# Optimization experiments

Hardware: AMD Instinct MI355X
Metric: run time of the kernel (lower is better)

## Reference

```python
import jax, jax.numpy as jnp
from jax import lax
import numpy as np

PRE_NMS_TOPN = 2000
POST_NMS_TOPN = 300
NMS_IOU_THRESHOLD = 0.7
EPS = 1e-8


def setup_inputs() -> dict:
    key = jax.random.key(0)
    k1, k2 = jax.random.split(key, 2)
    B, H, W, A = 64, 100, 100, 9
    # small-magnitude deltas so exp(dh/dw) stays sane, as real RPN outputs do
    rpn_bbox_deltas = jax.random.normal(k1, (B, H, W, A * 4), dtype=jnp.float32) * 0.1
    rpn_labels = jax.random.uniform(k2, (B, H, W, A), dtype=jnp.float32)
    # grid anchors, normalized coords, 3 scales x 3 ratios = 9 per position
    ys = (jnp.arange(H, dtype=jnp.float32) + 0.5) / H
    xs = (jnp.arange(W, dtype=jnp.float32) + 0.5) / W
    scales = jnp.array([0.1, 0.2, 0.4], dtype=jnp.float32)
    ratios = jnp.array([0.5, 1.0, 2.0], dtype=jnp.float32)
    hh = (scales[:, None] * jnp.sqrt(ratios)[None, :]).reshape(-1)  # [9]
    ww = (scales[:, None] / jnp.sqrt(ratios)[None, :]).reshape(-1)  # [9]
    cy, cx = jnp.meshgrid(ys, xs, indexing="ij")  # [H,W]
    cy, cx = cy[..., None], cx[..., None]         # [H,W,1]
    anchors = jnp.stack(
        [cy - hh / 2, cx - ww / 2, cy + hh / 2, cx + ww / 2], axis=-1
    ).reshape(-1, 4)  # [H*W*9, 4] = [90000, 4]
    return {"rpn_bbox_deltas": rpn_bbox_deltas, "rpn_labels": rpn_labels, "anchors": anchors}


def _decode_deltas(anchors, deltas):
    # anchors [N,4] (y1,x1,y2,x2), deltas [B,N,4] (dy,dx,dh,dw)
    anc_h = anchors[:, 2] - anchors[:, 0]
    anc_w = anchors[:, 3] - anchors[:, 1]
    anc_cy = anchors[:, 0] + 0.5 * anc_h
    anc_cx = anchors[:, 1] + 0.5 * anc_w
    h = jnp.exp(deltas[..., 2]) * anc_h
    w = jnp.exp(deltas[..., 3]) * anc_w
    cy = deltas[..., 0] * anc_h + anc_cy
    cx = deltas[..., 1] * anc_w + anc_cx
    y1 = cy - 0.5 * h
    x1 = cx - 0.5 * w
    return jnp.stack([y1, x1, y1 + h, x1 + w], axis=-1)  # [B,N,4]


def _nms_single(boxes):
    # boxes [PRE,4] already sorted by score descending; greedy hard NMS
    n = boxes.shape[0]
    area = jnp.maximum(boxes[:, 2] - boxes[:, 0], 0.0) * jnp.maximum(boxes[:, 3] - boxes[:, 1], 0.0)
    idx = jnp.arange(n)

    def body(i, keep):
        b = boxes[i]
        yy1 = jnp.maximum(b[0], boxes[:, 0])
        xx1 = jnp.maximum(b[1], boxes[:, 1])
        yy2 = jnp.minimum(b[2], boxes[:, 2])
        xx2 = jnp.minimum(b[3], boxes[:, 3])
        inter = jnp.maximum(yy2 - yy1, 0.0) * jnp.maximum(xx2 - xx1, 0.0)
        iou = inter / (area[i] + area - inter + EPS)
        suppress = (iou > NMS_IOU_THRESHOLD) & (idx > i) & keep[i]
        return keep & ~suppress

    keep = lax.fori_loop(0, n, body, jnp.ones((n,), dtype=bool))
    # compact kept boxes (score order) into fixed [POST,4], zero-padded
    pos = jnp.where(keep, jnp.cumsum(keep) - 1, POST_NMS_TOPN)
    pos = jnp.minimum(pos, POST_NMS_TOPN)
    out = jnp.zeros((POST_NMS_TOPN + 1, 4), dtype=boxes.dtype).at[pos].set(boxes)[:POST_NMS_TOPN]
    return jnp.clip(out, 0.0, 1.0)  # clip_boxes=True in tf combined NMS


def reference(rpn_bbox_deltas, rpn_labels, anchors):
    B = rpn_bbox_deltas.shape[0]
    N = anchors.shape[0]
    deltas = rpn_bbox_deltas.reshape(B, N, 4)
    labels = rpn_labels.reshape(B, N)
    boxes = _decode_deltas(anchors, deltas)             # [B,N,4]
    _, pre_idx = lax.top_k(labels, PRE_NMS_TOPN)        # [B,PRE] sorted desc
    pre_boxes = jnp.take_along_axis(boxes, pre_idx[..., None], axis=1)  # [B,PRE,4]
    roi_bboxes = jax.vmap(_nms_single)(pre_boxes)       # [B,POST,4]
    return lax.stop_gradient(roi_bboxes)
```

## Files before the change

kernel.cpp:

```cpp
#include <hip/hip_runtime.h>
#include <stdint.h>


#define PRE 2000
#define POST 300
#define TILE 512
#define IOU_THR 0.7f
#define EPSV 1e-8f
#define SORTN 2048
#define NBINS 2048
#define DESTCAP 4096
#define CANDCAP 512
#define CONS 1984
#define SL 16
#define KBUF 768

typedef unsigned long long u64;

__device__ __forceinline__ uint32_t flip_f32(uint32_t b) {
    return b ^ ((uint32_t)((int32_t)b >> 31) | 0x80000000u);
}

__device__ __forceinline__ int bin_of(float s) {
    int bn = (int)(s * 2048.0f);
    return min(max(bn, 0), NBINS - 1);
}

__device__ __forceinline__ u64 make_key(float s, int idx, int bn) {
    uint32_t ub = flip_f32(__float_as_uint(s));
    return ((u64)ub << 32) | ((uint32_t)bn << 20) |
           (uint32_t)(0xFFFFF - idx);
}

__device__ __forceinline__ bool iou_gt(const float4& bi, float ai,
                                       const float4& bj, float aj) {
    float yy1 = fmaxf(bi.x, bj.x);
    float xx1 = fmaxf(bi.y, bj.y);
    float yy2 = fminf(bi.z, bj.z);
    float xx2 = fminf(bi.w, bj.w);
    float inter = fmaxf(yy2 - yy1, 0.f) * fmaxf(xx2 - xx1, 0.f);
    float iou = inter / (ai + aj - inter + EPSV);
    return iou > IOU_THR;
}

__device__ __forceinline__ float area_of(const float4& bx) {
    return fmaxf(bx.z - bx.x, 0.f) * fmaxf(bx.w - bx.y, 0.f);
}

__device__ __forceinline__ u64 cs_keep(u64 v, u64 pv, int i, int j, int k) {
    bool lower   = ((i & j) == 0);
    bool desc    = ((i & k) == 0);
    bool keepmax = (desc == lower);
    u64 mx = v > pv ? v : pv;
    u64 mn = v > pv ? pv : v;
    return keepmax ? mx : mn;
}

__global__ __launch_bounds__(256) void k1_gather(
    const float4* __restrict__ score4,
    u64* __restrict__ g_pairs,
    int* __restrict__ g_scnt,
    int N)
{
    const int blk = blockIdx.x;
    const int b   = blk / SL;
    const int s   = blk % SL;
    const int tid = threadIdx.x;
    const int F4PB = N >> 2;
    const int F4PS = (F4PB + SL - 1) / SL;

    __shared__ u64 keybuf[KBUF];
    __shared__ int kcnt;

    if (tid == 0) kcnt = 0;
    __syncthreads();

    const float4* src = score4 + (size_t)b * F4PB;
    const int n0 = s * F4PS, n1 = min(n0 + F4PS, F4PB);
    for (int n = n0 + tid; n < n1; n += 256) {
        float4 v = src[n];
        float sv[4] = {v.x, v.y, v.z, v.w};
#pragma unroll
        for (int c = 0; c < 4; ++c) {
            int bn = bin_of(sv[c]);
            if (bn >= CONS) {
                int q = atomicAdd(&kcnt, 1);
                if (q < KBUF) keybuf[q] = make_key(sv[c], 4 * n + c, bn);
            }
        }
    }
    __syncthreads();

    if (tid == 0) g_scnt[b * SL + s] = kcnt;
    int lc = min(kcnt, KBUF);
    u64* gp = g_pairs + ((size_t)b * SL + s) * KBUF;
    for (int i = tid; i < lc; i += 256) gp[i] = keybuf[i];
}

__global__ __launch_bounds__(1024) void k2_sort(
    const float4* __restrict__ score4,
    const u64*  __restrict__ g_pairs,
    const int*  __restrict__ g_scnt,
    u64* __restrict__ g_sorted,
    int N)
{
    const int b    = blockIdx.x;
    const int tid  = threadIdx.x;
    const int lane = tid & 63;
    const int wv   = tid >> 6;

    __shared__ u64 dest[DESTCAP];
    __shared__ uint32_t hist2048[NBINS];
    __shared__ u64 cand[CANDCAP];
    __shared__ uint32_t hist64[64];
    __shared__ int segbase64[64];
    __shared__ uint32_t cur64[64];
    __shared__ int scnt_s[SL];
    __shared__ uint32_t wtot[16];
    __shared__ int sh_flag, sh_total, sh_bsel, sh_tprime, sh_cnt, sh_nc;
    __shared__ uint32_t sh_pivot;

    const int F4PB = N >> 2;

    if (tid < SL) scnt_s[tid] = g_scnt[b * SL + tid];
    if (tid < 64) { hist64[tid] = 0u; cur64[tid] = 0u; }
    if (tid == 0) { sh_flag = 0; sh_cnt = 0; sh_nc = 0; }
    __syncthreads();

    {
        int raw = scnt_s[wv];
        if (raw > KBUF) sh_flag = 1;
        int cs = min(raw, KBUF);
        const u64* gp = g_pairs + ((size_t)b * SL + wv) * KBUF;
        for (int i = lane; i < cs; i += 64) {
            int b64 = (int)((gp[i] >> 20) & 0xFFFu) - CONS;
            atomicAdd(&hist64[b64], 1u);
        }
    }
    __syncthreads();

    if (wv == 0) {
        int h = (int)hist64[lane];
        int ssum = h;
#pragma unroll
        for (int off = 1; off < 64; off <<= 1) {
            int t = __shfl_down(ssum, off, 64);
            if (lane + off < 64) ssum += t;
        }
        segbase64[lane] = ssum - h;
        if (lane == 0) sh_total = ssum;
        if (h > 128) sh_flag = 1;
    }
    __syncthreads();
    const int total = sh_total;
    if (tid == 0 && (total < PRE || total > DESTCAP)) sh_flag = 1;
    __syncthreads();
    const bool flag = (sh_flag != 0);

    if (!flag) {
        int cs = min(scnt_s[wv], KBUF);
        const u64* gp = g_pairs + ((size_t)b * SL + wv) * KBUF;
        for (int i = lane; i < cs; i += 64) {
            u64 key = gp[i];
            int b64 = (int)((key >> 20) & 0xFFFu) - CONS;
            int c = (int)atomicAdd(&cur64[b64], 1u);
            dest[segbase64[b64] + c] = key;
        }
        __syncthreads();
        for (int sgi = wv; sgi < 64; sgi += 16) {
            int n = (int)cur64[sgi];
            if (n <= 0) continue;
            int base = segbase64[sgi];
            if (n <= 64) {
                u64 e = (lane < n) ? dest[base + lane] : 0ull;
#pragma unroll
                for (int k = 2; k <= 64; k <<= 1)
                    for (int j = k >> 1; j > 0; j >>= 1)
                        e = cs_keep(e, __shfl_xor(e, j, 64), lane, j, k);
                if (lane < n) dest[base + lane] = e;
            } else {
                u64 e0 = (lane < n) ? dest[base + lane] : 0ull;
                u64 e1 = (lane + 64 < n) ? dest[base + lane + 64] : 0ull;
#pragma unroll
                for (int k = 2; k <= 128; k <<= 1) {
                    for (int j = k >> 1; j > 0; j >>= 1) {
                        if (j == 64) {
                            u64 a = e0, c = e1;
                            e0 = cs_keep(a, c, lane, 64, k);
                            e1 = cs_keep(c, a, lane + 64, 64, k);
                        } else {
                            e0 = cs_keep(e0, __shfl_xor(e0, j, 64), lane, j, k);
                            e1 = cs_keep(e1, __shfl_xor(e1, j, 64), lane + 64, j, k);
                        }
                    }
                }
                if (lane < n) dest[base + lane] = e0;
                if (lane + 64 < n) dest[base + lane + 64] = e1;
            }
        }
        __syncthreads();
        g_sorted[(size_t)b * SORTN + tid]        = dest[tid];
        g_sorted[(size_t)b * SORTN + tid + 1024] = dest[tid + 1024];
    } else {
        hist2048[tid] = 0u; hist2048[tid + 1024] = 0u;
        if (tid == 0) { sh_cnt = 0; sh_nc = 0; }
        __syncthreads();
        const float4* src = score4 + (size_t)b * F4PB;
        for (int n = tid; n < F4PB; n += 1024) {
            float4 v = src[n];
            atomicAdd(&hist2048[bin_of(v.x)], 1u);
            atomicAdd(&hist2048[bin_of(v.y)], 1u);
            atomicAdd(&hist2048[bin_of(v.z)], 1u);
            atomicAdd(&hist2048[bin_of(v.w)], 1u);
        }
        __syncthreads();
        {
            const int i0 = wv * 128 + lane;
            const int i1 = i0 + 64;
            int h0 = (int)hist2048[i0];
            int h1 = (int)hist2048[i1];
            int s0 = h0, s1 = h1;
#pragma unroll
            for (int off = 1; off < 64; off <<= 1) {
                int t0 = __shfl_down(s0, off, 64);
                int t1 = __shfl_down(s1, off, 64);
                if (lane + off < 64) { s0 += t0; s1 += t1; }
            }
            int sum_h1 = __shfl(s1, 0, 64);
            if (lane == 0) wtot[wv] = (uint32_t)(__shfl(s0, 0, 64) + sum_h1);
            __syncthreads();
            int offtot = 0;
            for (int w2 = wv + 1; w2 < 16; ++w2) offtot += (int)wtot[w2];
            int S0 = s0 + sum_h1 + offtot;
            int S1 = s1 + offtot;
            if (S0 >= PRE && S0 - h0 < PRE) { sh_bsel = i0; sh_tprime = PRE - (S0 - h0); }
            if (S1 >= PRE && S1 - h1 < PRE) { sh_bsel = i1; sh_tprime = PRE - (S1 - h1); }
        }
        __syncthreads();
        const int bsel   = sh_bsel;
        const int tprime = sh_tprime;
        for (int n = tid; n < F4PB; n += 1024) {
            float4 v = src[n];
            float sv[4] = {v.x, v.y, v.z, v.w};
#pragma unroll
            for (int c = 0; c < 4; ++c) {
                int bn = bin_of(sv[c]);
                if (bn >= bsel) {
                    u64 key = make_key(sv[c], 4 * n + c, bn);
                    if (bn > bsel) {
                        int q = atomicAdd(&sh_cnt, 1);
                        if (q < SORTN) dest[q] = key;
                    } else {
                        int t = atomicAdd(&sh_nc, 1);
                        if (t < CANDCAP) cand[t] = key;
                    }
                }
            }
        }
        __syncthreads();
        const int nc = min(sh_nc, CANDCAP);
        for (int i = tid; i < nc; i += 1024) {
            uint32_t vi = (uint32_t)(cand[i] >> 32);
            int g = 0, e = 0;
            for (int j = 0; j < nc; ++j) {
                uint32_t vj = (uint32_t)(cand[j] >> 32);
                g += (vj > vi);
                e += (vj == vi);
            }
            if (g < tprime && g + e >= tprime) sh_pivot = vi;
        }
        __syncthreads();
        const uint32_t pivot = sh_pivot;
        for (int i = tid; i < nc; i += 1024) {
            uint32_t vi = (uint32_t)(cand[i] >> 32);
            if (vi >= pivot) {
                int q = atomicAdd(&sh_cnt, 1);
                if (q < SORTN) dest[q] = cand[i];
            }
        }
        __syncthreads();
        const int tt = min(sh_cnt, SORTN);
        for (int q = tt + tid; q < SORTN; q += 1024) dest[q] = 0ull;
        __syncthreads();
        {
            const int i0 = wv * 128 + lane;
            const int i1 = i0 + 64;
            u64 e0 = dest[i0];
            u64 e1 = dest[i1];
            for (int k = 2; k <= SORTN; k <<= 1) {
                for (int j = k >> 1; j > 0; j >>= 1) {
                    if (j >= 128) {
                        dest[i0] = e0;
                        dest[i1] = e1;
                        __syncthreads();
                        u64 p0 = dest[i0 ^ j];
                        u64 p1 = dest[i1 ^ j];
                        __syncthreads();
                        e0 = cs_keep(e0, p0, i0, j, k);
                        e1 = cs_keep(e1, p1, i1, j, k);
                    } else if (j == 64) {
                        u64 a = e0, c = e1;
                        e0 = cs_keep(a, c, i0, 64, k);
                        e1 = cs_keep(c, a, i1, 64, k);
                    } else {
                        e0 = cs_keep(e0, __shfl_xor(e0, j, 64), i0, j, k);
                        e1 = cs_keep(e1, __shfl_xor(e1, j, 64), i1, j, k);
                    }
                }
            }
            g_sorted[(size_t)b * SORTN + i0] = e0;
            g_sorted[(size_t)b * SORTN + i1] = e1;
        }
    }
}

__global__ __launch_bounds__(256) void k3_decode(
    const float4* __restrict__ deltas,
    const float4* __restrict__ anchors,
    const u64*  __restrict__ g_sorted,
    float4* __restrict__ g_boxes,
    float*  __restrict__ g_area,
    int N)
{
    const int b   = blockIdx.x >> 2;
    const int s   = blockIdx.x & 3;
    const int tid = threadIdx.x;
    const int r0 = s * 512, r1 = min(r0 + 512, PRE);

    const float4* dl = deltas + (size_t)b * N;
    for (int r = r0 + tid; r < r1; r += 256) {
        u64 key = g_sorted[(size_t)b * SORTN + r];
        uint32_t idx = 0xFFFFFu - (uint32_t)(key & 0xFFFFFull);
        float4 bx = make_float4(0.f, 0.f, 0.f, 0.f);
        float  ar = 0.f;
        if (idx < (uint32_t)N) {
            float4 d  = dl[idx];
            float4 an = anchors[idx];
            float ah  = an.z - an.x;
            float aw  = an.w - an.y;
            float acy = an.x + 0.5f * ah;
            float acx = an.y + 0.5f * aw;
            float h   = expf(d.z) * ah;
            float w   = expf(d.w) * aw;
            float cy  = d.x * ah + acy;
            float cx  = d.y * aw + acx;
            float y1  = cy - 0.5f * h;
            float x1  = cx - 0.5f * w;
            bx = make_float4(y1, x1, y1 + h, x1 + w);
            ar = fmaxf(bx.z - bx.x, 0.f) * fmaxf(bx.w - bx.y, 0.f);
        }
        g_boxes[(size_t)b * PRE + r] = bx;
        g_area [(size_t)b * PRE + r] = ar;
    }
}

__global__ __launch_bounds__(256) void k4_supmat(
    const float4* __restrict__ g_boxes,
    uint32_t* __restrict__ g_supmat,
    uint32_t* __restrict__ g_supT)
{
    const int b   = blockIdx.x >> 4;
    const int s   = blockIdx.x & 15;
    const int tid = threadIdx.x;

    __shared__ float4 box[TILE];
    for (int i = tid; i < TILE; i += 256)
        box[i] = g_boxes[(size_t)b * PRE + i];
    __syncthreads();

    const int rbase = s * 32;
#pragma unroll
    for (int k = 0; k < 2; ++k) {
        int idx = tid + k * 256;
        int row = rbase + (idx & 31);
        int w   = idx >> 5;
        int jbase = w << 5;
        float4 bi = box[row];
        float  ai = area_of(bi);
        uint32_t bits = 0u;
        if (jbase + 31 > row) {
#pragma unroll
            for (int c = 0; c < 32; ++c) {
                int j = jbase + c;
                float4 bj = box[j];
                float  aj = area_of(bj);
                bool gt = (j > row) & iou_gt(bi, ai, bj, aj);
                bits |= ((uint32_t)gt) << c;
            }
        }
        g_supmat[((size_t)b * TILE + row) * 16 + w] = bits;
    }

    if (s < 8 && tid < 128) {
        int q  = s;
        int j  = tid >> 1;
        int w2 = tid & 1;
        int C  = q * 64 + j;
        float4 bc = box[C];
        float  ac = area_of(bc);
        uint32_t bits = 0u;
#pragma unroll
        for (int c = 0; c < 32; ++c) {
            int R = q * 64 + w2 * 32 + c;
            float4 br = box[R];
            float  ar = area_of(br);
            bool gt = (R < C) & iou_gt(br, ar, bc, ac);
            bits |= ((uint32_t)gt) << c;
        }
        g_supT[((size_t)b * TILE + C) * 2 + w2] = bits;
    }
}

__global__ __launch_bounds__(64) void k5_sweep(
    const uint32_t* __restrict__ g_supmat,
    const u64*    __restrict__ g_supT64,
    const float4* __restrict__ g_boxes,
    const float*  __restrict__ g_area,
    float4* __restrict__ out)
{
    const int b    = blockIdx.x;
    const int lane = threadIdx.x;

    __shared__ uint32_t kept[POST];
    __shared__ u64 sh_keepbits[TILE / 64];
    __shared__ uint32_t fmask[(PRE - TILE + 31) / 32];
    __shared__ int sh_kc;

    const u64* tdbase = g_supT64 + (size_t)b * TILE;

    uint32_t removedw = 0u;
    int kc = 0, nq = 0;
    u64 cw_cur = tdbase[lane];
    for (int q = 0; q < TILE / 64; ++q) {
        u64 cw_next = (q < TILE / 64 - 1) ? tdbase[(q + 1) * 64 + lane] : 0ull;
        const int cbase = q << 6;
        uint32_t rlo = (uint32_t)__builtin_amdgcn_readlane((int)removedw, 2 * q);
        uint32_t rhi = (uint32_t)__builtin_amdgcn_readlane((int)removedw, 2 * q + 1);
        u64 avail = ~(((u64)rhi << 32) | rlo);
        u64 K = 0ull;
        while (avail) {
            int i = __ffsll((long long)avail) - 1;
            K |= (1ull << i);
            u64 supp = __ballot(((cw_cur >> i) & 1ull) != 0ull);
            avail &= ~(supp | (1ull << i));
        }
        if (lane == 0) sh_keepbits[q] = K;
        kc += __popcll(K);
        nq = q + 1;
        if (kc >= POST) break;
        if (K) {
            const int w = lane & 15;
            const int g = lane >> 4;
            const uint32_t* gs =
                g_supmat + ((size_t)b * TILE + cbase + g * 16) * 16 + w;
            uint32_t acc = 0u;
#pragma unroll
            for (int r = 0; r < 16; ++r) {
                uint32_t v = gs[(size_t)r * 16];
                uint32_t m = (uint32_t)0 - (uint32_t)((K >> (g * 16 + r)) & 1ull);
                acc |= (v & m);
            }
            acc |= (uint32_t)__shfl_xor((int)acc, 16, 64);
            acc |= (uint32_t)__shfl_xor((int)acc, 32, 64);
            if (lane < 16) removedw |= acc;
        }
        cw_cur = cw_next;
    }
    {
        int base = 0;
        for (int q = 0; q < nq; ++q) {
            u64 kbq = sh_keepbits[q];
            int pos = base + __popcll(kbq & ((1ull << lane) - 1));
            if (((kbq >> lane) & 1ull) && pos < POST)
                kept[pos] = (uint32_t)(q * 64 + lane);
            base += __popcll(kbq);
        }
        if (lane == 0) sh_kc = min(kc, POST);
    }
    __syncthreads();
    int kcf = sh_kc;

    if (kcf < POST) {
        for (int w = lane; w < (PRE - TILE + 31) / 32; w += 64) fmask[w] = 0u;
        __syncthreads();
        for (int j = TILE + lane; j < PRE; j += 64) {
            float4 bj = g_boxes[(size_t)b * PRE + j];
            float  aj = g_area [(size_t)b * PRE + j];
            bool supd = false;
            for (int k = 0; k < kcf; ++k) {
                int i = (int)kept[k];
                float4 bi = g_boxes[(size_t)b * PRE + i];
                float  ai = g_area [(size_t)b * PRE + i];
                if (iou_gt(bi, ai, bj, aj)) { supd = true; break; }
            }
            if (supd) atomicOr(&fmask[(j - TILE) >> 5], 1u << ((j - TILE) & 31));
        }
        __syncthreads();
        int i = TILE;
        while (i < PRE && kcf < POST) {
            while (i < PRE && ((fmask[(i - TILE) >> 5] >> ((i - TILE) & 31)) & 1u)) ++i;
            if (i >= PRE) break;
            if (lane == 0) kept[kcf] = (uint32_t)i;
            ++kcf;
            if (kcf >= POST) break;
            float4 bi = g_boxes[(size_t)b * PRE + i];
            float  ai = g_area [(size_t)b * PRE + i];
            for (int j = i + 1 + lane; j < PRE; j += 64) {
                float4 bj = g_boxes[(size_t)b * PRE + j];
                float  aj = g_area [(size_t)b * PRE + j];
                if (iou_gt(bi, ai, bj, aj))
                    atomicOr(&fmask[(j - TILE) >> 5], 1u << ((j - TILE) & 31));
            }
            ++i;
            __syncthreads();
        }
    }
    __syncthreads();

    float4* ob = out + (size_t)b * POST;
    for (int r = lane; r < POST; r += 64) {
        float4 o = make_float4(0.f, 0.f, 0.f, 0.f);
        if (r < kcf) {
            float4 bx = g_boxes[(size_t)b * PRE + kept[r]];
            o.x = fminf(fmaxf(bx.x, 0.f), 1.f);
            o.y = fminf(fmaxf(bx.y, 0.f), 1.f);
            o.z = fminf(fmaxf(bx.z, 0.f), 1.f);
            o.w = fminf(fmaxf(bx.w, 0.f), 1.f);
        }
        ob[r] = o;
    }
}

extern "C" void kernel_launch(void* const* d_in, const int* in_sizes, int n_in,
                              void* d_out, int out_size, void* d_ws, size_t ws_size,
                              hipStream_t stream) {
    const float4* deltas  = (const float4*)d_in[0];
    const float*  labels  = (const float*)d_in[1];
    const float4* anchors = (const float4*)d_in[2];
    const float4* score4  = (const float4*)labels;
    float4*       outp    = (float4*)d_out;
    const int N = in_sizes[2] / 4;
    const int B = in_sizes[1] / N;

    char* ws = (char*)d_ws;
    const size_t SZ_BOXES  = (size_t)B * PRE * 16;
    const size_t SZ_PAIRS  = (size_t)B * SL * KBUF * 8;
    const size_t SZ_SORTED = (size_t)B * SORTN * 8;
    const size_t SZ_SUPMAT = (size_t)B * TILE * 16 * 4;
    const size_t SZ_SUPT   = (size_t)B * TILE * 8;
    const size_t SZ_AREA   = (size_t)B * PRE * 4;
    float4*   g_boxes  = (float4*)ws;
    u64*      g_pairs  = (u64*)(ws + SZ_BOXES);
    u64*      g_sorted = (u64*)(ws + SZ_BOXES + SZ_PAIRS);
    uint32_t* g_supmat = (uint32_t*)(ws + SZ_BOXES + SZ_PAIRS + SZ_SORTED);
    uint32_t* g_supT   = (uint32_t*)(ws + SZ_BOXES + SZ_PAIRS + SZ_SORTED + SZ_SUPMAT);
    float*    g_area   = (float*)(ws + SZ_BOXES + SZ_PAIRS + SZ_SORTED + SZ_SUPMAT + SZ_SUPT);
    int*      g_scnt   = (int*)(ws + SZ_BOXES + SZ_PAIRS + SZ_SORTED + SZ_SUPMAT + SZ_SUPT + SZ_AREA);

    k1_gather<<<B * SL, 256, 0, stream>>>(score4, g_pairs, g_scnt, N);
    k2_sort<<<B, 1024, 0, stream>>>(score4, g_pairs, g_scnt, g_sorted, N);
    k3_decode<<<B * 4, 256, 0, stream>>>(deltas, anchors, g_sorted,
                                         g_boxes, g_area, N);
    k4_supmat<<<B * 16, 256, 0, stream>>>(g_boxes, g_supmat, g_supT);
    k5_sweep<<<B, 64, 0, stream>>>(g_supmat, (const u64*)g_supT,
                                   g_boxes, g_area, outp);
}
```

Measured before the change: 80.90 us.

## Fuse box decode into suppression-matrix kernel and pre-bin keys in gather

Removes the separate decode kernel. Each suppression-matrix block now decodes its 512 top boxes straight from the sorted keys, and the sweep kernel decodes all 2000 boxes into shared memory only when it falls back. The gather kernel also buckets its keys by sub-bin and writes per-slice histograms, so the sort kernel can scatter with computed offsets instead of re-histogramming and using shared atomics. This saves one launch and global round trips, at the cost of redundant decode work across the 16 blocks per batch and more shared memory in the gather and sweep kernels.

```diff
diff --git a/kernel.cpp b/kernel.cpp
--- a/kernel.cpp
+++ b/kernel.cpp
@@ -47,6 +47,25 @@
     return fmaxf(bx.z - bx.x, 0.f) * fmaxf(bx.w - bx.y, 0.f);
 }
 
+__device__ __forceinline__ float4 decode_key(u64 key, const float4* dl,
+                                             const float4* anchors, int N) {
+    uint32_t idx = 0xFFFFFu - (uint32_t)(key & 0xFFFFFull);
+    if (idx >= (uint32_t)N) return make_float4(0.f, 0.f, 0.f, 0.f);
+    float4 d  = dl[idx];
+    float4 an = anchors[idx];
+    float ah  = an.z - an.x;
+    float aw  = an.w - an.y;
+    float acy = an.x + 0.5f * ah;
+    float acx = an.y + 0.5f * aw;
+    float h   = expf(d.z) * ah;
+    float w   = expf(d.w) * aw;
+    float cy  = d.x * ah + acy;
+    float cx  = d.y * aw + acx;
+    float y1  = cy - 0.5f * h;
+    float x1  = cx - 0.5f * w;
+    return make_float4(y1, x1, y1 + h, x1 + w);
+}
+
 __device__ __forceinline__ u64 cs_keep(u64 v, u64 pv, int i, int j, int k) {
     bool lower   = ((i & j) == 0);
     bool desc    = ((i & k) == 0);
@@ -60,18 +79,25 @@
     const float4* __restrict__ score4,
     u64* __restrict__ g_pairs,
     int* __restrict__ g_scnt,
+    uint32_t* __restrict__ g_shist,
     int N)
 {
     const int blk = blockIdx.x;
     const int b   = blk / SL;
     const int s   = blk % SL;
     const int tid = threadIdx.x;
+    const int lane = tid & 63;
     const int F4PB = N >> 2;
     const int F4PS = (F4PB + SL - 1) / SL;
 
     __shared__ u64 keybuf[KBUF];
+    __shared__ u64 binbuf[KBUF];
+    __shared__ uint32_t hist64[64];
+    __shared__ int base64[64];
+    __shared__ uint32_t cur64[64];
     __shared__ int kcnt;
 
+    if (tid < 64) { hist64[tid] = 0u; cur64[tid] = 0u; }
     if (tid == 0) kcnt = 0;
     __syncthreads();
 
@@ -91,16 +117,46 @@
     }
     __syncthreads();
 
-    if (tid == 0) g_scnt[b * SL + s] = kcnt;
-    int lc = min(kcnt, KBUF);
+    const int raw = kcnt;
+    const int lc  = min(raw, KBUF);
+
+    for (int i = tid; i < lc; i += 256) {
+        int b64 = (int)((keybuf[i] >> 20) & 0xFFFu) - CONS;
+        atomicAdd(&hist64[b64], 1u);
+    }
+    __syncthreads();
+
+    if (tid < 64) {
+        int h = (int)hist64[lane];
+        int ssum = h;
+#pragma unroll
+        for (int off = 1; off < 64; off <<= 1) {
+            int t = __shfl_down(ssum, off, 64);
+            if (lane + off < 64) ssum += t;
+        }
+        base64[lane] = ssum - h;
+    }
+    __syncthreads();
+
+    for (int i = tid; i < lc; i += 256) {
+        u64 key = keybuf[i];
+        int b64 = (int)((key >> 20) & 0xFFFu) - CONS;
+        int p = (int)atomicAdd(&cur64[b64], 1u);
+        binbuf[base64[b64] + p] = key;
+    }
+    __syncthreads();
+
+    if (tid == 0) g_scnt[b * SL + s] = raw;
+    if (tid < 64) g_shist[((size_t)b * SL + s) * 64 + tid] = hist64[tid];
     u64* gp = g_pairs + ((size_t)b * SL + s) * KBUF;
-    for (int i = tid; i < lc; i += 256) gp[i] = keybuf[i];
+    for (int i = tid; i < lc; i += 256) gp[i] = binbuf[i];
 }
 
 __global__ __launch_bounds__(1024) void k2_sort(
     const float4* __restrict__ score4,
     const u64*  __restrict__ g_pairs,
     const int*  __restrict__ g_scnt,
+    const uint32_t* __restrict__ g_shist,
     u64* __restrict__ g_sorted,
     int N)
 {
@@ -112,63 +168,81 @@
     __shared__ u64 dest[DESTCAP];
     __shared__ uint32_t hist2048[NBINS];
     __shared__ u64 cand[CANDCAP];
-    __shared__ uint32_t hist64[64];
+    __shared__ uint32_t shist[SL][64];
+    __shared__ int srcb[SL][64];
+    __shared__ int sbase[SL][64];
+    __shared__ int tot64[64];
     __shared__ int segbase64[64];
-    __shared__ uint32_t cur64[64];
-    __shared__ int scnt_s[SL];
     __shared__ uint32_t wtot[16];
     __shared__ int sh_flag, sh_total, sh_bsel, sh_tprime, sh_cnt, sh_nc;
     __shared__ uint32_t sh_pivot;
 
     const int F4PB = N >> 2;
 
-    if (tid < SL) scnt_s[tid] = g_scnt[b * SL + tid];
-    if (tid < 64) { hist64[tid] = 0u; cur64[tid] = 0u; }
-    if (tid == 0) { sh_flag = 0; sh_cnt = 0; sh_nc = 0; }
-    __syncthreads();
-
+    shist[tid >> 6][tid & 63] = g_shist[(size_t)b * SL * 64 + tid];
+    if (tid == 0) {
+        int f = 0;
+#pragma unroll
+        for (int s = 0; s < SL; ++s)
+            if (g_scnt[b * SL + s] > KBUF) f = 1;
+        sh_flag = f;
+    }
+    __syncthreads();
+
+    if (tid < 64) {
+        int acc = 0;
+#pragma unroll
+        for (int s = 0; s < SL; ++s) acc += (int)shist[s][tid];
+        tot64[tid] = acc;
+        if (acc > 128) sh_flag = 1;
+    }
     {
-        int raw = scnt_s[wv];
-        if (raw > KBUF) sh_flag = 1;
-        int cs = min(raw, KBUF);
-        const u64* gp = g_pairs + ((size_t)b * SL + wv) * KBUF;
-        for (int i = lane; i < cs; i += 64) {
-            int b64 = (int)((gp[i] >> 20) & 0xFFFu) - CONS;
-            atomicAdd(&hist64[b64], 1u);
-        }
-    }
-    __syncthreads();
-
-    if (wv == 0) {
-        int h = (int)hist64[lane];
+        int h = (int)shist[wv][lane];
         int ssum = h;
 #pragma unroll
         for (int off = 1; off < 64; off <<= 1) {
             int t = __shfl_down(ssum, off, 64);
             if (lane + off < 64) ssum += t;
         }
-        segbase64[lane] = ssum - h;
+        srcb[wv][lane] = ssum - h;
+    }
+    __syncthreads();
+
+    if (tid < 64) {
+        int t0 = tot64[lane];
+        int ssum = t0;
+#pragma unroll
+        for (int off = 1; off < 64; off <<= 1) {
+            int t = __shfl_down(ssum, off, 64);
+            if (lane + off < 64) ssum += t;
+        }
+        segbase64[lane] = ssum - t0;
         if (lane == 0) sh_total = ssum;
-        if (h > 128) sh_flag = 1;
     }
     __syncthreads();
     const int total = sh_total;
     if (tid == 0 && (total < PRE || total > DESTCAP)) sh_flag = 1;
+    {
+        int s   = tid >> 6;
+        int b64 = tid & 63;
+        int pre = 0;
+        for (int s2 = 0; s2 < s; ++s2) pre += (int)shist[s2][b64];
+        sbase[s][b64] = segbase64[b64] + pre;
+    }
     __syncthreads();
     const bool flag = (sh_flag != 0);
 
     if (!flag) {
-        int cs = min(scnt_s[wv], KBUF);
+        const int cs = min(g_scnt[b * SL + wv], KBUF);
         const u64* gp = g_pairs + ((size_t)b * SL + wv) * KBUF;
         for (int i = lane; i < cs; i += 64) {
             u64 key = gp[i];
             int b64 = (int)((key >> 20) & 0xFFFu) - CONS;
-            int c = (int)atomicAdd(&cur64[b64], 1u);
-            dest[segbase64[b64] + c] = key;
+            dest[sbase[wv][b64] + (i - srcb[wv][b64])] = key;
         }
         __syncthreads();
         for (int sgi = wv; sgi < 64; sgi += 16) {
-            int n = (int)cur64[sgi];
+            int n = tot64[sgi];
             if (n <= 0) continue;
             int base = segbase64[sgi];
             if (n <= 64) {
@@ -314,59 +388,36 @@
     }
 }
 
-__global__ __launch_bounds__(256) void k3_decode(
+__global__ __launch_bounds__(256) void k4_supmat(
     const float4* __restrict__ deltas,
     const float4* __restrict__ anchors,
     const u64*  __restrict__ g_sorted,
     float4* __restrict__ g_boxes,
-    float*  __restrict__ g_area,
+    uint32_t* __restrict__ g_supmat,
+    uint32_t* __restrict__ g_supT,
     int N)
-{
-    const int b   = blockIdx.x >> 2;
-    const int s   = blockIdx.x & 3;
-    const int tid = threadIdx.x;
-    const int r0 = s * 512, r1 = min(r0 + 512, PRE);
-
-    const float4* dl = deltas + (size_t)b * N;
-    for (int r = r0 + tid; r < r1; r += 256) {
-        u64 key = g_sorted[(size_t)b * SORTN + r];
-        uint32_t idx = 0xFFFFFu - (uint32_t)(key & 0xFFFFFull);
-        float4 bx = make_float4(0.f, 0.f, 0.f, 0.f);
-        float  ar = 0.f;
-        if (idx < (uint32_t)N) {
-            float4 d  = dl[idx];
-            float4 an = anchors[idx];
-            float ah  = an.z - an.x;
-            float aw  = an.w - an.y;
-            float acy = an.x + 0.5f * ah;
-            float acx = an.y + 0.5f * aw;
-            float h   = expf(d.z) * ah;
-            float w   = expf(d.w) * aw;
-            float cy  = d.x * ah + acy;
-            float cx  = d.y * aw + acx;
-            float y1  = cy - 0.5f * h;
-            float x1  = cx - 0.5f * w;
-            bx = make_float4(y1, x1, y1 + h, x1 + w);
-            ar = fmaxf(bx.z - bx.x, 0.f) * fmaxf(bx.w - bx.y, 0.f);
-        }
-        g_boxes[(size_t)b * PRE + r] = bx;
-        g_area [(size_t)b * PRE + r] = ar;
-    }
-}
-
-__global__ __launch_bounds__(256) void k4_supmat(
-    const float4* __restrict__ g_boxes,
-    uint32_t* __restrict__ g_supmat,
-    uint32_t* __restrict__ g_supT)
 {
     const int b   = blockIdx.x >> 4;
     const int s   = blockIdx.x & 15;
     const int tid = threadIdx.x;
 
     __shared__ float4 box[TILE];
-    for (int i = tid; i < TILE; i += 256)
-        box[i] = g_boxes[(size_t)b * PRE + i];
-    __syncthreads();
+
+    const float4* dl = deltas + (size_t)b * N;
+#pragma unroll
+    for (int k = 0; k < 2; ++k) {
+        int r = tid + k * 256;
+        box[r] = decode_key(g_sorted[(size_t)b * SORTN + r], dl, anchors, N);
+    }
+    __syncthreads();
+
+    if (s == 0) {
+#pragma unroll
+        for (int k = 0; k < 2; ++k) {
+            int r = tid + k * 256;
+            g_boxes[(size_t)b * TILE + r] = box[r];
+        }
+    }
 
     const int rbase = s * 32;
 #pragma unroll
@@ -414,17 +465,22 @@
 __global__ __launch_bounds__(64) void k5_sweep(
     const uint32_t* __restrict__ g_supmat,
     const u64*    __restrict__ g_supT64,
+    const u64*    __restrict__ g_sorted,
+    const float4* __restrict__ deltas,
+    const float4* __restrict__ anchors,
     const float4* __restrict__ g_boxes,
-    const float*  __restrict__ g_area,
-    float4* __restrict__ out)
+    float4* __restrict__ out,
+    int N)
 {
     const int b    = blockIdx.x;
     const int lane = threadIdx.x;
 
     __shared__ uint32_t kept[POST];
     __shared__ u64 sh_keepbits[TILE / 64];
+    __shared__ int sh_kc;
+    __shared__ float4 fbox[PRE];
+    __shared__ float  farea[PRE];
     __shared__ uint32_t fmask[(PRE - TILE + 31) / 32];
-    __shared__ int sh_kc;
 
     const u64* tdbase = g_supT64 + (size_t)b * TILE;
 
@@ -479,19 +535,25 @@
     }
     __syncthreads();
     int kcf = sh_kc;
-
-    if (kcf < POST) {
+    const bool fellback = (kcf < POST);
+
+    if (fellback) {
+        const float4* dl = deltas + (size_t)b * N;
+        for (int r = lane; r < PRE; r += 64) {
+            float4 bx = decode_key(g_sorted[(size_t)b * SORTN + r], dl,
+                                   anchors, N);
+            fbox[r]  = bx;
+            farea[r] = area_of(bx);
+        }
         for (int w = lane; w < (PRE - TILE + 31) / 32; w += 64) fmask[w] = 0u;
         __syncthreads();
         for (int j = TILE + lane; j < PRE; j += 64) {
-            float4 bj = g_boxes[(size_t)b * PRE + j];
-            float  aj = g_area [(size_t)b * PRE + j];
+            float4 bj = fbox[j];
+            float  aj = farea[j];
             bool supd = false;
             for (int k = 0; k < kcf; ++k) {
                 int i = (int)kept[k];
-                float4 bi = g_boxes[(size_t)b * PRE + i];
-                float  ai = g_area [(size_t)b * PRE + i];
-                if (iou_gt(bi, ai, bj, aj)) { supd = true; break; }
+                if (iou_gt(fbox[i], farea[i], bj, aj)) { supd = true; break; }
             }
             if (supd) atomicOr(&fmask[(j - TILE) >> 5], 1u << ((j - TILE) & 31));
         }
@@ -503,12 +565,10 @@
             if (lane == 0) kept[kcf] = (uint32_t)i;
             ++kcf;
             if (kcf >= POST) break;
-            float4 bi = g_boxes[(size_t)b * PRE + i];
-            float  ai = g_area [(size_t)b * PRE + i];
+            float4 bi = fbox[i];
+            float  ai = farea[i];
             for (int j = i + 1 + lane; j < PRE; j += 64) {
-                float4 bj = g_boxes[(size_t)b * PRE + j];
-                float  aj = g_area [(size_t)b * PRE + j];
-                if (iou_gt(bi, ai, bj, aj))
+                if (iou_gt(bi, ai, fbox[j], farea[j]))
                     atomicOr(&fmask[(j - TILE) >> 5], 1u << ((j - TILE) & 31));
             }
             ++i;
@@ -521,7 +581,9 @@
     for (int r = lane; r < POST; r += 64) {
         float4 o = make_float4(0.f, 0.f, 0.f, 0.f);
         if (r < kcf) {
-            float4 bx = g_boxes[(size_t)b * PRE + kept[r]];
+            int ki = (int)kept[r];
+            float4 bx = fellback ? fbox[ki]
+                                 : g_boxes[(size_t)b * TILE + ki];
             o.x = fminf(fmaxf(bx.x, 0.f), 1.f);
             o.y = fminf(fmaxf(bx.y, 0.f), 1.f);
             o.z = fminf(fmaxf(bx.z, 0.f), 1.f);
@@ -543,25 +605,25 @@
     const int B = in_sizes[1] / N;
 
     char* ws = (char*)d_ws;
-    const size_t SZ_BOXES  = (size_t)B * PRE * 16;
+    const size_t SZ_BOXES  = (size_t)B * TILE * 16;
     const size_t SZ_PAIRS  = (size_t)B * SL * KBUF * 8;
     const size_t SZ_SORTED = (size_t)B * SORTN * 8;
     const size_t SZ_SUPMAT = (size_t)B * TILE * 16 * 4;
     const size_t SZ_SUPT   = (size_t)B * TILE * 8;
-    const size_t SZ_AREA   = (size_t)B * PRE * 4;
+    const size_t SZ_SHIST  = (size_t)B * SL * 64 * 4;
     float4*   g_boxes  = (float4*)ws;
     u64*      g_pairs  = (u64*)(ws + SZ_BOXES);
     u64*      g_sorted = (u64*)(ws + SZ_BOXES + SZ_PAIRS);
     uint32_t* g_supmat = (uint32_t*)(ws + SZ_BOXES + SZ_PAIRS + SZ_SORTED);
     uint32_t* g_supT   = (uint32_t*)(ws + SZ_BOXES + SZ_PAIRS + SZ_SORTED + SZ_SUPMAT);
-    float*    g_area   = (float*)(ws + SZ_BOXES + SZ_PAIRS + SZ_SORTED + SZ_SUPMAT + SZ_SUPT);
-    int*      g_scnt   = (int*)(ws + SZ_BOXES + SZ_PAIRS + SZ_SORTED + SZ_SUPMAT + SZ_SUPT + SZ_AREA);
-
-    k1_gather<<<B * SL, 256, 0, stream>>>(score4, g_pairs, g_scnt, N);
-    k2_sort<<<B, 1024, 0, stream>>>(score4, g_pairs, g_scnt, g_sorted, N);
-    k3_decode<<<B * 4, 256, 0, stream>>>(deltas, anchors, g_sorted,
-                                         g_boxes, g_area, N);
-    k4_supmat<<<B * 16, 256, 0, stream>>>(g_boxes, g_supmat, g_supT);
-    k5_sweep<<<B, 64, 0, stream>>>(g_supmat, (const u64*)g_supT,
-                                   g_boxes, g_area, outp);
-}
+    uint32_t* g_shist  = (uint32_t*)(ws + SZ_BOXES + SZ_PAIRS + SZ_SORTED + SZ_SUPMAT + SZ_SUPT);
+    int*      g_scnt   = (int*)((char*)g_shist + SZ_SHIST);
+
+    k1_gather<<<B * SL, 256, 0, stream>>>(score4, g_pairs, g_scnt, g_shist, N);
+    k2_sort<<<B, 1024, 0, stream>>>(score4, g_pairs, g_scnt, g_shist,
+                                    g_sorted, N);
+    k4_supmat<<<B * 16, 256, 0, stream>>>(deltas, anchors, g_sorted,
+                                          g_boxes, g_supmat, g_supT, N);
+    k5_sweep<<<B, 64, 0, stream>>>(g_supmat, (const u64*)g_supT, g_sorted,
+                                   deltas, anchors, g_boxes, outp, N);
+}
```

After: 75.68 us (median of 3 runs). 6.5% less time.
